# Kernel tuning notes

Measured on AMD Instinct MI355X. Metric: run time of the kernel, lower is better.

Reference implementation:

```python
import jax, jax.numpy as jnp
import numpy as np

N_NODES = 100000

def setup_inputs() -> dict:
    key = jax.random.key(0)
    k = jax.random.split(key, 6)
    d, dout = 128, 128
    x = jax.random.normal(k[0], (N_NODES, d), dtype=jnp.float32)
    edge_index = jax.random.randint(k[1], (2, 3200000), 0, N_NODES, dtype=jnp.int64)
    s = 1.0 / np.sqrt(d)
    W1 = jax.random.uniform(k[2], (d, d), jnp.float32, -s, s)
    b1 = jnp.zeros((d,), jnp.float32)
    W2 = jax.random.uniform(k[3], (d, d), jnp.float32, -s, s)
    b2 = jnp.zeros((d,), jnp.float32)
    W3 = jax.random.uniform(k[4], (d, dout), jnp.float32, -s, s)
    b3 = jnp.zeros((dout,), jnp.float32)
    return {"x": x, "W1": W1, "b1": b1, "W2": W2, "b2": b2, "W3": W3, "b3": b3, "edge_index": edge_index}

def reference(x, W1, b1, W2, b2, W3, b3, edge_index):
    src, dst = edge_index[0], edge_index[1]
    # GINConv aggregation: sum of neighbor features into destination nodes
    agg = jax.ops.segment_sum(x[src], dst, num_segments=N_NODES)  # [N, d]
    h = x + agg  # (1 + eps)*x + agg, eps = 0 (PyG default)
    # MLP1: linear1 -> ReLU -> linear2 -> ReLU
    h = jax.nn.relu(h @ W1 + b1)
    h = jax.nn.relu(h @ W2 + b2)
    # linear3 -> ReLU
    out = jax.nn.relu(h @ W3 + b3)
    return out
```

## Files before the change

### kernel.cpp

```cpp
#include <hip/hip_runtime.h>

#define N_NODES 100000
#define D 128
#define E_EDGES 3200000
#define BSHIFT 8
#define NPB 256
#define NBIN 391
#define BCAP 8960
#define PBLK 512
#define CHUNK (E_EDGES / PBLK)

typedef short bf16x8 __attribute__((ext_vector_type(8)));
typedef float f32x4 __attribute__((ext_vector_type(4)));

__device__ __forceinline__ unsigned rne_bf16(float f) {
    unsigned u = __float_as_uint(f);
    return (u + 0x7FFFu + ((u >> 16) & 1u)) >> 16;
}

__global__ __launch_bounds__(256) void w_prep(const float* __restrict__ W1,
                                              const float* __restrict__ W2,
                                              const float* __restrict__ W3,
                                              unsigned short* __restrict__ wt,
                                              int* __restrict__ ctrl) {
    int e = blockIdx.x * 256 + threadIdx.x;
    if (e < 1024) ctrl[e] = 0;
    if (e < 3 * 16384) {
        int l = e >> 14, r = e & 16383;
        int k = r >> 7, n = r & 127;
        const float* W = l == 0 ? W1 : (l == 1 ? W2 : W3);
        wt[l * 16384 + n * 128 + k] = (unsigned short)rne_bf16(W[r]);
    }
}

__global__ __launch_bounds__(256) void to_bf16(const float* __restrict__ x,
                                               unsigned* __restrict__ xb) {
    int i = blockIdx.x * 256 + threadIdx.x;
    float2 v = ((const float2*)x)[i];
    xb[i] = rne_bf16(v.x) | (rne_bf16(v.y) << 16);
}

__global__ __launch_bounds__(256) void partition_edges(const int* __restrict__ eidx,
                                                       int* __restrict__ gcnt,
                                                       unsigned* __restrict__ bbuf) {
    __shared__ int ssrc[CHUNK];
    __shared__ int sdst[CHUNK];
    __shared__ int hist[NBIN];
    __shared__ int cur[NBIN];
    int tid = threadIdx.x;
    for (int i = tid; i < NBIN; i += 256) hist[i] = 0;
    __syncthreads();
    int e0 = blockIdx.x * CHUNK;
    for (int i = tid; i < CHUNK; i += 256) {
        int s = eidx[e0 + i];
        int d = eidx[E_EDGES + e0 + i];
        ssrc[i] = s;
        sdst[i] = d;
        atomicAdd(&hist[d >> BSHIFT], 1);
    }
    __syncthreads();
    for (int b = tid; b < NBIN; b += 256)
        cur[b] = atomicAdd(&gcnt[b], hist[b]);
    __syncthreads();
    for (int i = tid; i < CHUNK; i += 256) {
        int d = sdst[i];
        int b = d >> BSHIFT;
        int slot = atomicAdd(&cur[b], 1);
        if (slot < BCAP)
            bbuf[(size_t)b * BCAP + slot] = ((unsigned)(d & 255) << 17) | (unsigned)ssrc[i];
    }
}

__global__ __launch_bounds__(256) void build_csr(const int* __restrict__ gcnt,
                                                 const unsigned* __restrict__ bbuf,
                                                 int* __restrict__ gpos,
                                                 int* __restrict__ col,
                                                 int2* __restrict__ meta) {
    __shared__ unsigned ebuf[BCAP];
    __shared__ int hist[NPB], pre[NPB], cur[NPB];
    __shared__ int sh_base;
    int b = blockIdx.x, tid = threadIdx.x;
    int mb = min(gcnt[b], BCAP);
    hist[tid] = 0;
    cur[tid] = 0;
    __syncthreads();
    for (int i = tid; i < mb; i += 256) {
        unsigned w = bbuf[(size_t)b * BCAP + i];
        ebuf[i] = w;
        atomicAdd(&hist[w >> 17], 1);
    }
    __syncthreads();
    if (tid < 64) {
        int a0 = hist[tid * 4 + 0], a1 = hist[tid * 4 + 1];
        int a2 = hist[tid * 4 + 2], a3 = hist[tid * 4 + 3];
        int s = a0 + a1 + a2 + a3;
        int t = s;
        for (int off = 1; off < 64; off <<= 1) {
            int v = __shfl_up(t, off, 64);
            if (tid >= off) t += v;
        }
        int excl = t - s;
        pre[tid * 4 + 0] = excl;
        pre[tid * 4 + 1] = excl + a0;
        pre[tid * 4 + 2] = excl + a0 + a1;
        pre[tid * 4 + 3] = excl + a0 + a1 + a2;
    }
    if (tid == 0) sh_base = atomicAdd(gpos, mb);
    __syncthreads();
    int gbase = sh_base;
    for (int i = tid; i < mb; i += 256) {
        unsigned w = ebuf[i];
        int l = (int)(w >> 17);
        int slot = atomicAdd(&cur[l], 1);
        col[gbase + pre[l] + slot] = (int)(w & 0x1FFFFu);
    }
    __syncthreads();
    int n = (b << BSHIFT) + tid;
    if (n < N_NODES) meta[n] = make_int2(gbase + pre[tid], hist[tid]);
}

__global__ __launch_bounds__(256) void gather_h0(const float* __restrict__ x,
                                                 const unsigned* __restrict__ xb,
                                                 const int2* __restrict__ meta,
                                                 const int* __restrict__ col,
                                                 unsigned* __restrict__ h0b) {
    int lane = threadIdx.x & 63;
    int n = __builtin_amdgcn_readfirstlane(blockIdx.x * 4 + (threadIdx.x >> 6));
    int2 mt = meta[n];
    int base = mt.x, m = mt.y;
    float2 acc = ((const float2*)x)[n * 64 + lane];
    for (int c = 0; c < m; c += 64) {
        int rem = m - c;
        int lim = rem < 64 ? rem : 64;
        int idx = 0;
        if (lane < lim) idx = col[base + c + lane];
        int j = 0;
        for (; j + 16 <= lim; j += 16) {
            unsigned u[16];
#pragma unroll
            for (int q = 0; q < 16; ++q) {
                int s = __shfl(idx, j + q, 64);
                u[q] = xb[s * 64 + lane];
            }
#pragma unroll
            for (int q = 0; q < 16; ++q) {
                acc.x += __uint_as_float(u[q] << 16);
                acc.y += __uint_as_float(u[q] & 0xFFFF0000u);
            }
        }
        for (; j + 4 <= lim; j += 4) {
            unsigned u[4];
#pragma unroll
            for (int q = 0; q < 4; ++q) {
                int s = __shfl(idx, j + q, 64);
                u[q] = xb[s * 64 + lane];
            }
#pragma unroll
            for (int q = 0; q < 4; ++q) {
                acc.x += __uint_as_float(u[q] << 16);
                acc.y += __uint_as_float(u[q] & 0xFFFF0000u);
            }
        }
        for (; j < lim; ++j) {
            int s = __shfl(idx, j, 64);
            unsigned u = xb[s * 64 + lane];
            acc.x += __uint_as_float(u << 16);
            acc.y += __uint_as_float(u & 0xFFFF0000u);
        }
    }
    h0b[n * 64 + lane] = rne_bf16(acc.x) | (rne_bf16(acc.y) << 16);
}

#define HBW 136

__global__ __launch_bounds__(256, 4) void mlp_mfma(const unsigned* __restrict__ h0b,
                                                   float* __restrict__ out,
                                                   const unsigned short* __restrict__ wt,
                                                   const float* __restrict__ b1,
                                                   const float* __restrict__ b2,
                                                   const float* __restrict__ b3) {
    __shared__ unsigned short hb[128 * HBW];
    int tid = threadIdx.x;
    int w = tid >> 6, lane = tid & 63;
    int m = lane & 15, quad = lane >> 4;
    int r0 = blockIdx.x * 128 + w * 32;

    for (int it = 0; it < 8; ++it) {
        int flat = it * 64 + lane;
        int lr = flat >> 4, c4 = flat & 15;
        int gr = r0 + lr; if (gr >= N_NODES) gr = N_NODES - 1;
        uint4 v = ((const uint4*)h0b)[gr * 16 + c4];
        *(uint4*)&hb[(w * 32 + lr) * HBW + c4 * 8] = v;
    }

    const float* bias[3] = {b1, b2, b3};
    for (int l = 0; l < 3; ++l) {
        const unsigned short* W = wt + l * 16384;
        float bv[8];
#pragma unroll
        for (int ct = 0; ct < 8; ++ct) bv[ct] = bias[l][ct * 16 + m];

        f32x4 acc[2][8];
#pragma unroll
        for (int rt = 0; rt < 2; ++rt)
#pragma unroll
            for (int ct = 0; ct < 8; ++ct) acc[rt][ct] = (f32x4){0.f, 0.f, 0.f, 0.f};

#pragma unroll
        for (int ks = 0; ks < 4; ++ks) {
            bf16x8 a0 = *(const bf16x8*)&hb[(w * 32 + m) * HBW + ks * 32 + quad * 8];
            bf16x8 a1 = *(const bf16x8*)&hb[(w * 32 + 16 + m) * HBW + ks * 32 + quad * 8];
#pragma unroll
            for (int ct = 0; ct < 8; ++ct) {
                bf16x8 bf = *(const bf16x8*)&W[(ct * 16 + m) * 128 + ks * 32 + quad * 8];
                acc[0][ct] = __builtin_amdgcn_mfma_f32_16x16x32_bf16(a0, bf, acc[0][ct], 0, 0, 0);
                acc[1][ct] = __builtin_amdgcn_mfma_f32_16x16x32_bf16(a1, bf, acc[1][ct], 0, 0, 0);
            }
        }

        if (l < 2) {
#pragma unroll
            for (int rt = 0; rt < 2; ++rt)
#pragma unroll
                for (int ct = 0; ct < 8; ++ct)
#pragma unroll
                    for (int r = 0; r < 4; ++r) {
                        float v = acc[rt][ct][r] + bv[ct];
                        v = v > 0.f ? v : 0.f;
                        hb[(w * 32 + rt * 16 + quad * 4 + r) * HBW + ct * 16 + m] =
                            (unsigned short)rne_bf16(v);
                    }
        } else {
#pragma unroll
            for (int rt = 0; rt < 2; ++rt)
#pragma unroll
                for (int r = 0; r < 4; ++r) {
                    int gr = r0 + rt * 16 + quad * 4 + r;
                    if (gr < N_NODES) {
#pragma unroll
                        for (int ct = 0; ct < 8; ++ct) {
                            float v = acc[rt][ct][r] + bv[ct];
                            out[(size_t)gr * 128 + ct * 16 + m] = v > 0.f ? v : 0.f;
                        }
                    }
                }
        }
    }
}

extern "C" void kernel_launch(void* const* d_in, const int* in_sizes, int n_in,
                              void* d_out, int out_size, void* d_ws, size_t ws_size,
                              hipStream_t stream) {
    const float* x  = (const float*)d_in[0];
    const float* W1 = (const float*)d_in[1];
    const float* b1 = (const float*)d_in[2];
    const float* W2 = (const float*)d_in[3];
    const float* b2 = (const float*)d_in[4];
    const float* W3 = (const float*)d_in[5];
    const float* b3 = (const float*)d_in[6];
    const int*  eidx = (const int*)d_in[7];
    float* out = (float*)d_out;

    const size_t OFF_WT   = 4096;
    const size_t OFF_META = OFF_WT + 98304;
    const size_t OFF_COL  = OFF_META + 800256;
    const size_t OFF_BBUF = OFF_COL + (size_t)E_EDGES * 4;

    int* ctrl = (int*)d_ws;
    int* gcnt = (int*)d_ws;
    int* gpos = (int*)((char*)d_ws + 2048);
    unsigned short* wtb = (unsigned short*)((char*)d_ws + OFF_WT);
    int2* meta = (int2*)((char*)d_ws + OFF_META);
    int* col = (int*)((char*)d_ws + OFF_COL);
    unsigned* bbuf = (unsigned*)((char*)d_ws + OFF_BBUF);
    unsigned* h0b = bbuf;
    unsigned* xb = (unsigned*)d_out;

    w_prep<<<192, 256, 0, stream>>>(W1, W2, W3, wtb, ctrl);
    to_bf16<<<(N_NODES * D / 2) / 256, 256, 0, stream>>>(x, xb);
    partition_edges<<<PBLK, 256, 0, stream>>>(eidx, gcnt, bbuf);
    build_csr<<<NBIN, 256, 0, stream>>>(gcnt, bbuf, gpos, col, meta);
    gather_h0<<<N_NODES / 4, 256, 0, stream>>>(x, xb, meta, col, h0b);
    mlp_mfma<<<(N_NODES + 127) / 128, 256, 0, stream>>>(h0b, out, wtb, b1, b2, b3);
}
```

Measured before the change: 349.2 us.

## Vectorize neighbor gather with 16-byte loads and fuse prep kernels

```diff
diff --git a/kernel.cpp b/kernel.cpp
--- a/kernel.cpp
+++ b/kernel.cpp
@@ -7,8 +7,8 @@
 #define NPB 256
 #define NBIN 391
 #define BCAP 8960
-#define PBLK 512
-#define CHUNK (E_EDGES / PBLK)
+#define PBLK 625
+#define CHUNK 5120
 
 typedef short bf16x8 __attribute__((ext_vector_type(8)));
 typedef float f32x4 __attribute__((ext_vector_type(4)));
@@ -17,27 +17,26 @@
     unsigned u = __float_as_uint(f);
     return (u + 0x7FFFu + ((u >> 16) & 1u)) >> 16;
 }
-
-__global__ __launch_bounds__(256) void w_prep(const float* __restrict__ W1,
-                                              const float* __restrict__ W2,
-                                              const float* __restrict__ W3,
-                                              unsigned short* __restrict__ wt,
-                                              int* __restrict__ ctrl) {
-    int e = blockIdx.x * 256 + threadIdx.x;
-    if (e < 1024) ctrl[e] = 0;
-    if (e < 3 * 16384) {
-        int l = e >> 14, r = e & 16383;
+__device__ __forceinline__ float bf_lo(unsigned u) { return __uint_as_float(u << 16); }
+__device__ __forceinline__ float bf_hi(unsigned u) { return __uint_as_float(u & 0xFFFF0000u); }
+
+__global__ __launch_bounds__(256) void prep(const float* __restrict__ x,
+                                            const float* __restrict__ W1,
+                                            const float* __restrict__ W2,
+                                            const float* __restrict__ W3,
+                                            unsigned* __restrict__ xb,
+                                            unsigned short* __restrict__ wt,
+                                            int* __restrict__ ctrl) {
+    int i = blockIdx.x * 256 + threadIdx.x;
+    float2 v = ((const float2*)x)[i];
+    xb[i] = rne_bf16(v.x) | (rne_bf16(v.y) << 16);
+    if (i < 1024) ctrl[i] = 0;
+    if (i < 3 * 16384) {
+        int l = i >> 14, r = i & 16383;
         int k = r >> 7, n = r & 127;
         const float* W = l == 0 ? W1 : (l == 1 ? W2 : W3);
         wt[l * 16384 + n * 128 + k] = (unsigned short)rne_bf16(W[r]);
     }
-}
-
-__global__ __launch_bounds__(256) void to_bf16(const float* __restrict__ x,
-                                               unsigned* __restrict__ xb) {
-    int i = blockIdx.x * 256 + threadIdx.x;
-    float2 v = ((const float2*)x)[i];
-    xb[i] = rne_bf16(v.x) | (rne_bf16(v.y) << 16);
 }
 
 __global__ __launch_bounds__(256) void partition_edges(const int* __restrict__ eidx,
@@ -51,23 +50,38 @@
     for (int i = tid; i < NBIN; i += 256) hist[i] = 0;
     __syncthreads();
     int e0 = blockIdx.x * CHUNK;
-    for (int i = tid; i < CHUNK; i += 256) {
-        int s = eidx[e0 + i];
-        int d = eidx[E_EDGES + e0 + i];
-        ssrc[i] = s;
-        sdst[i] = d;
-        atomicAdd(&hist[d >> BSHIFT], 1);
+    const int4* s4 = (const int4*)(eidx + e0);
+    const int4* d4 = (const int4*)(eidx + E_EDGES + e0);
+#pragma unroll
+    for (int it = 0; it < 5; ++it) {
+        int i = it * 256 + tid;
+        int4 s = s4[i], d = d4[i];
+        ((int4*)ssrc)[i] = s;
+        ((int4*)sdst)[i] = d;
+        atomicAdd(&hist[d.x >> BSHIFT], 1);
+        atomicAdd(&hist[d.y >> BSHIFT], 1);
+        atomicAdd(&hist[d.z >> BSHIFT], 1);
+        atomicAdd(&hist[d.w >> BSHIFT], 1);
     }
     __syncthreads();
     for (int b = tid; b < NBIN; b += 256)
         cur[b] = atomicAdd(&gcnt[b], hist[b]);
     __syncthreads();
-    for (int i = tid; i < CHUNK; i += 256) {
-        int d = sdst[i];
-        int b = d >> BSHIFT;
-        int slot = atomicAdd(&cur[b], 1);
-        if (slot < BCAP)
-            bbuf[(size_t)b * BCAP + slot] = ((unsigned)(d & 255) << 17) | (unsigned)ssrc[i];
+#pragma unroll
+    for (int it = 0; it < 5; ++it) {
+        int i = it * 256 + tid;
+        int4 s = ((const int4*)ssrc)[i];
+        int4 d = ((const int4*)sdst)[i];
+        int sv[4] = {s.x, s.y, s.z, s.w};
+        int dv[4] = {d.x, d.y, d.z, d.w};
+#pragma unroll
+        for (int q = 0; q < 4; ++q) {
+            int b = dv[q] >> BSHIFT;
+            int slot = atomicAdd(&cur[b], 1);
+            if (slot < BCAP)
+                bbuf[(size_t)b * BCAP + slot] =
+                    ((unsigned)(dv[q] & 255) << 17) | (unsigned)sv[q];
+        }
     }
 }
 
@@ -119,16 +133,30 @@
     if (n < N_NODES) meta[n] = make_int2(gbase + pre[tid], hist[tid]);
 }
 
-__global__ __launch_bounds__(256) void gather_h0(const float* __restrict__ x,
-                                                 const unsigned* __restrict__ xb,
+__global__ __launch_bounds__(256) void gather_h0(const unsigned* __restrict__ xb,
                                                  const int2* __restrict__ meta,
                                                  const int* __restrict__ col,
                                                  unsigned* __restrict__ h0b) {
     int lane = threadIdx.x & 63;
     int n = __builtin_amdgcn_readfirstlane(blockIdx.x * 4 + (threadIdx.x >> 6));
+    int g = lane >> 4;
+    int li = lane & 15;
     int2 mt = meta[n];
     int base = mt.x, m = mt.y;
-    float2 acc = ((const float2*)x)[n * 64 + lane];
+
+    const uint4* xb4 = (const uint4*)xb;
+    float acc[8];
+    if (g == 0) {
+        uint4 sv = xb4[n * 16 + li];
+        acc[0] = bf_lo(sv.x); acc[1] = bf_hi(sv.x);
+        acc[2] = bf_lo(sv.y); acc[3] = bf_hi(sv.y);
+        acc[4] = bf_lo(sv.z); acc[5] = bf_hi(sv.z);
+        acc[6] = bf_lo(sv.w); acc[7] = bf_hi(sv.w);
+    } else {
+#pragma unroll
+        for (int k = 0; k < 8; ++k) acc[k] = 0.f;
+    }
+
     for (int c = 0; c < m; c += 64) {
         int rem = m - c;
         int lim = rem < 64 ? rem : 64;
@@ -136,39 +164,53 @@
         if (lane < lim) idx = col[base + c + lane];
         int j = 0;
         for (; j + 16 <= lim; j += 16) {
-            unsigned u[16];
-#pragma unroll
-            for (int q = 0; q < 16; ++q) {
-                int s = __shfl(idx, j + q, 64);
-                u[q] = xb[s * 64 + lane];
+            uint4 u[4];
+#pragma unroll
+            for (int t = 0; t < 4; ++t) {
+                int s = __shfl(idx, j + t * 4 + g, 64);
+                u[t] = xb4[s * 16 + li];
             }
 #pragma unroll
-            for (int q = 0; q < 16; ++q) {
-                acc.x += __uint_as_float(u[q] << 16);
-                acc.y += __uint_as_float(u[q] & 0xFFFF0000u);
+            for (int t = 0; t < 4; ++t) {
+                acc[0] += bf_lo(u[t].x); acc[1] += bf_hi(u[t].x);
+                acc[2] += bf_lo(u[t].y); acc[3] += bf_hi(u[t].y);
+                acc[4] += bf_lo(u[t].z); acc[5] += bf_hi(u[t].z);
+                acc[6] += bf_lo(u[t].w); acc[7] += bf_hi(u[t].w);
             }
         }
         for (; j + 4 <= lim; j += 4) {
-            unsigned u[4];
-#pragma unroll
-            for (int q = 0; q < 4; ++q) {
-                int s = __shfl(idx, j + q, 64);
-                u[q] = xb[s * 64 + lane];
+            int s = __shfl(idx, j + g, 64);
+            uint4 u = xb4[s * 16 + li];
+            acc[0] += bf_lo(u.x); acc[1] += bf_hi(u.x);
+            acc[2] += bf_lo(u.y); acc[3] += bf_hi(u.y);
+            acc[4] += bf_lo(u.z); acc[5] += bf_hi(u.z);
+            acc[6] += bf_lo(u.w); acc[7] += bf_hi(u.w);
+        }
+        int tail = lim - j;
+        if (tail > 0) {
+            int s = __shfl(idx, j + (g < tail ? g : 0), 64);
+            if (g < tail) {
+                uint4 u = xb4[s * 16 + li];
+                acc[0] += bf_lo(u.x); acc[1] += bf_hi(u.x);
+                acc[2] += bf_lo(u.y); acc[3] += bf_hi(u.y);
+                acc[4] += bf_lo(u.z); acc[5] += bf_hi(u.z);
+                acc[6] += bf_lo(u.w); acc[7] += bf_hi(u.w);
             }
-#pragma unroll
-            for (int q = 0; q < 4; ++q) {
-                acc.x += __uint_as_float(u[q] << 16);
-                acc.y += __uint_as_float(u[q] & 0xFFFF0000u);
-            }
-        }
-        for (; j < lim; ++j) {
-            int s = __shfl(idx, j, 64);
-            unsigned u = xb[s * 64 + lane];
-            acc.x += __uint_as_float(u << 16);
-            acc.y += __uint_as_float(u & 0xFFFF0000u);
-        }
-    }
-    h0b[n * 64 + lane] = rne_bf16(acc.x) | (rne_bf16(acc.y) << 16);
+        }
+    }
+#pragma unroll
+    for (int k = 0; k < 8; ++k) {
+        acc[k] += __shfl_xor(acc[k], 16, 64);
+        acc[k] += __shfl_xor(acc[k], 32, 64);
+    }
+    if (g == 0) {
+        uint4 o;
+        o.x = rne_bf16(acc[0]) | (rne_bf16(acc[1]) << 16);
+        o.y = rne_bf16(acc[2]) | (rne_bf16(acc[3]) << 16);
+        o.z = rne_bf16(acc[4]) | (rne_bf16(acc[5]) << 16);
+        o.w = rne_bf16(acc[6]) | (rne_bf16(acc[7]) << 16);
+        ((uint4*)h0b)[n * 16 + li] = o;
+    }
 }
 
 #define HBW 136
@@ -276,10 +318,9 @@
     unsigned* h0b = bbuf;
     unsigned* xb = (unsigned*)d_out;
 
-    w_prep<<<192, 256, 0, stream>>>(W1, W2, W3, wtb, ctrl);
-    to_bf16<<<(N_NODES * D / 2) / 256, 256, 0, stream>>>(x, xb);
+    prep<<<25000, 256, 0, stream>>>(x, W1, W2, W3, xb, wtb, ctrl);
     partition_edges<<<PBLK, 256, 0, stream>>>(eidx, gcnt, bbuf);
     build_csr<<<NBIN, 256, 0, stream>>>(gcnt, bbuf, gpos, col, meta);
-    gather_h0<<<N_NODES / 4, 256, 0, stream>>>(x, xb, meta, col, h0b);
+    gather_h0<<<N_NODES / 4, 256, 0, stream>>>(xb, meta, col, h0b);
     mlp_mfma<<<(N_NODES + 127) / 128, 256, 0, stream>>>(h0b, out, wtb, b1, b2, b3);
 }
```

New measurement: 337.2 us. 1.04x faster.
